# Performance work log

Hardware: AMD Instinct MI355X
Metric: run time of the kernel (lower is better)

The kernel has to match this reference:

```python
import jax, jax.numpy as jnp
import numpy as np

N_NODES = 50000
N_EDGES = 800000
D = 256


def _mean_aggregate(x, src, tgt, num_nodes):
    # scatter-mean of source features onto target nodes: [N, D]
    summed = jax.ops.segment_sum(x[src], tgt, num_segments=num_nodes)
    count = jax.ops.segment_sum(jnp.ones((src.shape[0],), x.dtype), tgt,
                                num_segments=num_nodes)
    return summed / jnp.maximum(count, 1.0)[:, None]


def _sage_conv(x, src, tgt, W_l, b, W_r):
    # PyG SAGEConv (aggr='mean'): lin_l(mean_j x_j) + lin_r(x_i)
    agg = _mean_aggregate(x, src, tgt, x.shape[0])
    return agg @ W_l + b + x @ W_r


def setup_inputs() -> dict:
    key = jax.random.key(0)
    ks = jax.random.split(key, 8)
    s = 1.0 / np.sqrt(D)
    x = jax.random.normal(ks[0], (N_NODES, D), dtype=jnp.float32)
    edge_index = jax.random.randint(ks[1], (2, N_EDGES), 0, N_NODES, dtype=jnp.int64)
    return {
        "x": x,
        "edge_index": edge_index,
        "W1_l": jax.random.normal(ks[2], (D, D), dtype=jnp.float32) * s,
        "b1": jnp.zeros((D,), dtype=jnp.float32),
        "W1_r": jax.random.normal(ks[3], (D, D), dtype=jnp.float32) * s,
        "W2_l": jax.random.normal(ks[4], (D, D), dtype=jnp.float32) * s,
        "b2": jnp.zeros((D,), dtype=jnp.float32),
        "W2_r": jax.random.normal(ks[5], (D, D), dtype=jnp.float32) * s,
    }


def reference(x, edge_index, W1_l, b1, W1_r, W2_l, b2, W2_r):
    src, tgt = edge_index[0], edge_index[1]
    h = jax.nn.relu(_sage_conv(x, src, tgt, W1_l, b1, W1_r))
    return _sage_conv(h, src, tgt, W2_l, b2, W2_r)
```

## Files before the change

### kernel.cpp

```cpp
#include <hip/hip_runtime.h>
#include <hip/hip_bf16.h>

#define NN 50000
#define NE 800000
#define DD 256
#define KK 512
#define PAD 64
#define CSTR 16

#define FB 3125
#define CB 12500
#define WB 1024

typedef unsigned short u16;
typedef unsigned int   u32;
typedef unsigned char  u8;
typedef __attribute__((ext_vector_type(8))) __bf16 bf16x8;
typedef __attribute__((ext_vector_type(4))) float  f32x4;
typedef __attribute__((ext_vector_type(2))) float  f32x2;
typedef __attribute__((ext_vector_type(8))) u16    u16x8;
typedef __attribute__((ext_vector_type(4))) u16    u16x4;

#define GLOAD_LDS16(g, l) \
  __builtin_amdgcn_global_load_lds((const __attribute__((address_space(1))) void*)(g), \
                                   (__attribute__((address_space(3))) void*)(l), 16, 0, 0)

static __device__ __forceinline__ u16 f2bf(float f) {
  u32 u = __float_as_uint(f);
  u32 r = (u + 0x7FFFu + ((u >> 16) & 1u)) >> 16;
  return (u16)r;
}
static __device__ __forceinline__ float bf2f(u16 h) {
  return __uint_as_float(((u32)h) << 16);
}

__global__ void k_prep(const int* __restrict__ src, const int* __restrict__ tgt,
                       int* __restrict__ cnt, int* __restrict__ col,
                       const float* __restrict__ x, u16* __restrict__ x_bf,
                       u32* __restrict__ x_f8,
                       const float* __restrict__ W1l, const float* __restrict__ W1r,
                       const float* __restrict__ W2l, const float* __restrict__ W2r,
                       u16* __restrict__ Wc1T, u16* __restrict__ Wc2T) {
  const int b = blockIdx.x;
  if (b < FB) {
    int i = b * 256 + threadIdx.x;
    int t = tgt[i];
    int p = atomicAdd(&cnt[t * CSTR], 1);
    if (p < PAD) col[t * PAD + p] = src[i];
  } else if (b < FB + CB) {
    int i = (b - FB) * 256 + threadIdx.x;
    const float4 v = *reinterpret_cast<const float4*>(x + i * 4);
    u16x4 o; o.x = f2bf(v.x); o.y = f2bf(v.y); o.z = f2bf(v.z); o.w = f2bf(v.w);
    *reinterpret_cast<u16x4*>(x_bf + i * 4) = o;
    int pk = __builtin_amdgcn_cvt_pk_fp8_f32(v.x, v.y, 0, false);
    pk = __builtin_amdgcn_cvt_pk_fp8_f32(v.z, v.w, pk, true);
    x_f8[i] = (u32)pk;
  } else {
    int gid = (b - FB - CB) * 256 + threadIdx.x;
    int layer = gid >> 17;
    int idx = gid & 131071;
    int n = idx >> 9, k = idx & 511;
    const float* Wl = layer ? W2l : W1l;
    const float* Wr = layer ? W2r : W1r;
    u16* WcT = layer ? Wc2T : Wc1T;
    float v = (k < DD) ? Wl[k * DD + n] : Wr[(k - DD) * DD + n];
    int reg = k >> 6, ko = k & 63;
    int k2 = (reg << 6) + ((((ko >> 3) ^ (n & 7)) << 3)) + (ko & 7);
    WcT[n * KK + k2] = f2bf(v);
  }
}

__global__ void k_aggregate(const u8* __restrict__ feat8, const int* __restrict__ cnt,
                            const int* __restrict__ col, u16* __restrict__ out) {
  const int wave = threadIdx.x >> 6;
  const int lane = threadIdx.x & 63;
  const int half = lane >> 5;
  const int l32 = lane & 31;
  const int node = blockIdx.x * 4 + wave;
  int deg = cnt[node * CSTR];
  if (deg > PAD) deg = PAD;
  const int s = node * PAD, e = s + deg;
  const int fo = l32 * 8;
  float a[8] = {0.f, 0.f, 0.f, 0.f, 0.f, 0.f, 0.f, 0.f};

#define ACC8(vv)                                                       \
  {                                                                    \
    f32x2 p0 = __builtin_amdgcn_cvt_pk_f32_fp8((int)(vv).x, false);    \
    f32x2 p1 = __builtin_amdgcn_cvt_pk_f32_fp8((int)(vv).x, true);     \
    f32x2 p2 = __builtin_amdgcn_cvt_pk_f32_fp8((int)(vv).y, false);    \
    f32x2 p3 = __builtin_amdgcn_cvt_pk_f32_fp8((int)(vv).y, true);     \
    a[0] += p0.x; a[1] += p0.y; a[2] += p1.x; a[3] += p1.y;            \
    a[4] += p2.x; a[5] += p2.y; a[6] += p3.x; a[7] += p3.y;            \
  }

  int i = s + half;
  for (; i + 6 < e; i += 8) {
    int c0 = col[i], c1 = col[i + 2], c2 = col[i + 4], c3 = col[i + 6];
    uint2 v0 = *reinterpret_cast<const uint2*>(feat8 + c0 * DD + fo);
    uint2 v1 = *reinterpret_cast<const uint2*>(feat8 + c1 * DD + fo);
    uint2 v2 = *reinterpret_cast<const uint2*>(feat8 + c2 * DD + fo);
    uint2 v3 = *reinterpret_cast<const uint2*>(feat8 + c3 * DD + fo);
    ACC8(v0) ACC8(v1) ACC8(v2) ACC8(v3)
  }
  for (; i < e; i += 2) {
    uint2 v = *reinterpret_cast<const uint2*>(feat8 + col[i] * DD + fo);
    ACC8(v)
  }
#undef ACC8
#pragma unroll
  for (int j = 0; j < 8; ++j) a[j] += __shfl_xor(a[j], 32, 64);

  if (half == 0) {
    const float scale = (deg > 0) ? 1.0f / (float)deg : 0.0f;
    u16x8 o;
#pragma unroll
    for (int j = 0; j < 8; ++j) o[j] = f2bf(a[j] * scale);
    *reinterpret_cast<u16x8*>(out + node * DD + fo) = o;
  }
}

#define BM 64
#define BN 256
#define BK 64

template <int LAYER>
__global__ void k_gemm_fused(const u16* __restrict__ A0, const u16* __restrict__ A1,
                             const u16* __restrict__ WcT, const float* __restrict__ bias,
                             u16* __restrict__ outb, u8* __restrict__ outf8,
                             float* __restrict__ outf, int M) {
  __shared__ alignas(16) u16 lA[BM * BK];
  __shared__ alignas(16) u16 lB[BN * BK];
  const int tid = threadIdx.x;
  const int rowBase = blockIdx.x * BM;
  const int wave = tid >> 6, lane = tid & 63;
  const int wc = wave;
  const int l8 = lane >> 3;
  const int ch = lane & 7;

  f32x4 acc[4][4] = {};

  for (int k0 = 0; k0 < KK; k0 += BK) {
    if (k0) __syncthreads();
    const u16* Asrc = (k0 < DD) ? A0 : A1;
    const int kk = k0 & (DD - 1);
#pragma unroll
    for (int j = 0; j < 2; ++j) {
      int row = wave * 16 + j * 8 + l8;
      const u16* g = Asrc + (size_t)(rowBase + row) * DD + kk + ((ch ^ (row & 7)) << 3);
      GLOAD_LDS16(g, &lA[(wave * 16 + j * 8) * BK]);
    }
#pragma unroll
    for (int j = 0; j < 8; ++j) {
      int row = wave * 64 + j * 8 + l8;
      const u16* g = WcT + (size_t)row * KK + k0 + (ch << 3);
      GLOAD_LDS16(g, &lB[(wave * 64 + j * 8) * BK]);
    }
    __syncthreads();

#pragma unroll
    for (int ks = 0; ks < 2; ++ks) {
      const int kbyte = ks * 64 + (lane >> 4) * 16;
      bf16x8 af[4], bfg[4];
#pragma unroll
      for (int m = 0; m < 4; ++m) {
        int row = m * 16 + (lane & 15);
        af[m] = *reinterpret_cast<const bf16x8*>((const char*)lA + row * 128 + (kbyte ^ ((row & 7) << 4)));
      }
#pragma unroll
      for (int n = 0; n < 4; ++n) {
        int row = wc * 64 + n * 16 + (lane & 15);
        bfg[n] = *reinterpret_cast<const bf16x8*>((const char*)lB + row * 128 + (kbyte ^ ((row & 7) << 4)));
      }
#pragma unroll
      for (int m = 0; m < 4; ++m)
#pragma unroll
        for (int n = 0; n < 4; ++n)
          acc[m][n] = __builtin_amdgcn_mfma_f32_16x16x32_bf16(af[m], bfg[n], acc[m][n], 0, 0, 0);
    }
  }

  const int lrow = (lane >> 4) * 4;
  const int lcol = lane & 15;
#pragma unroll
  for (int n = 0; n < 4; ++n) {
    const int gcol = wc * 64 + n * 16 + lcol;
    const float bv = bias[gcol];
#pragma unroll
    for (int m = 0; m < 4; ++m) {
#pragma unroll
      for (int r = 0; r < 4; ++r) {
        const int grow = rowBase + m * 16 + lrow + r;
        if (grow < M) {
          float v = acc[m][n][r] + bv;
          if (LAYER == 1) {
            v = fmaxf(v, 0.0f);
            outb[grow * DD + gcol] = f2bf(v);
            int pk = __builtin_amdgcn_cvt_pk_fp8_f32(v, 0.0f, 0, false);
            outf8[grow * DD + gcol] = (u8)(pk & 0xff);
          } else {
            outf[grow * DD + gcol] = v;
          }
        }
      }
    }
  }
}

extern "C" void kernel_launch(void* const* d_in, const int* in_sizes, int n_in,
                              void* d_out, int out_size, void* d_ws, size_t ws_size,
                              hipStream_t stream) {
  const float* x    = (const float*)d_in[0];
  const int*   ei   = (const int*)d_in[1];
  const float* W1l  = (const float*)d_in[2];
  const float* b1   = (const float*)d_in[3];
  const float* W1r  = (const float*)d_in[4];
  const float* W2l  = (const float*)d_in[5];
  const float* b2   = (const float*)d_in[6];
  const float* W2r  = (const float*)d_in[7];
  float* out = (float*)d_out;

  const int* srcIdx = ei;
  const int* tgtIdx = ei + NE;

  char* ws = (char*)d_ws;
  int* cnt    = (int*)(ws + 0);
  int* col    = (int*)(ws + 3200000);
  u16* x_bf   = (u16*)(ws + 16000000);
  u16* h_bf   = (u16*)(ws + 41600000);
  u16* agg_bf = (u16*)(ws + 67200000);
  u8*  x_f8   = (u8*) (ws + 92800000);
  u8*  h_f8   = (u8*) (ws + 105600000);
  u16* Wc1T   = (u16*)(ws + 118400000);
  u16* Wc2T   = (u16*)(ws + 118662144);

  hipMemsetAsync(cnt, 0, NN * CSTR * sizeof(int), stream);
  k_prep<<<FB + CB + WB, 256, 0, stream>>>(srcIdx, tgtIdx, cnt, col, x, x_bf,
                                           (u32*)x_f8,
                                           W1l, W1r, W2l, W2r, Wc1T, Wc2T);

  const int ggrid = (NN + BM - 1) / BM;

  k_aggregate<<<NN / 4, 256, 0, stream>>>(x_f8, cnt, col, agg_bf);
  k_gemm_fused<1><<<ggrid, 256, 0, stream>>>(agg_bf, x_bf, Wc1T, b1, h_bf, h_f8, nullptr, NN);
  k_aggregate<<<NN / 4, 256, 0, stream>>>(h_f8, cnt, col, agg_bf);
  k_gemm_fused<2><<<ggrid, 256, 0, stream>>>(agg_bf, h_bf, Wc2T, b2, nullptr, nullptr, out, NN);
}
```

Measured before the change: 199.6 us.

## Bucket edges by target range then build padded CSR with LDS atomics

Replaces the per-edge global atomic on a strided count array with a two-pass bucketing scheme. Edges are first binned into 7 target-range buckets, each split into 32 replicas, using wave-aggregated atomics. A new 56-block kernel then scans its bucket's replicas and fills the padded adjacency using shared-memory counters. This removes 800k contended global atomics and the large memset. The cost is an extra kernel launch, an extra write and read of an 8-byte edge buffer, and each build block rescanning its whole bucket. Segment capacity overflow could silently drop edges if the distribution is skewed.

```diff
diff --git a/kernel.cpp b/kernel.cpp
--- a/kernel.cpp
+++ b/kernel.cpp
@@ -6,7 +6,11 @@
 #define DD 256
 #define KK 512
 #define PAD 64
-#define CSTR 16
+
+#define NBUCK 7
+#define BSH 13
+#define REPL 32
+#define SEGCAP 5120
 
 #define FB 3125
 #define CB 12500
@@ -15,6 +19,7 @@
 typedef unsigned short u16;
 typedef unsigned int   u32;
 typedef unsigned char  u8;
+typedef unsigned long long u64;
 typedef __attribute__((ext_vector_type(8))) __bf16 bf16x8;
 typedef __attribute__((ext_vector_type(4))) float  f32x4;
 typedef __attribute__((ext_vector_type(2))) float  f32x2;
@@ -30,12 +35,9 @@
   u32 r = (u + 0x7FFFu + ((u >> 16) & 1u)) >> 16;
   return (u16)r;
 }
-static __device__ __forceinline__ float bf2f(u16 h) {
-  return __uint_as_float(((u32)h) << 16);
-}
 
 __global__ void k_prep(const int* __restrict__ src, const int* __restrict__ tgt,
-                       int* __restrict__ cnt, int* __restrict__ col,
+                       int* __restrict__ cur, u64* __restrict__ ebuf,
                        const float* __restrict__ x, u16* __restrict__ x_bf,
                        u32* __restrict__ x_f8,
                        const float* __restrict__ W1l, const float* __restrict__ W1r,
@@ -43,10 +45,25 @@
                        u16* __restrict__ Wc1T, u16* __restrict__ Wc2T) {
   const int b = blockIdx.x;
   if (b < FB) {
-    int i = b * 256 + threadIdx.x;
-    int t = tgt[i];
-    int p = atomicAdd(&cnt[t * CSTR], 1);
-    if (p < PAD) col[t * PAD + p] = src[i];
+    const int i = b * 256 + threadIdx.x;
+    const int lane = threadIdx.x & 63;
+    const int t = tgt[i], s = src[i];
+    const int bk = t >> BSH;
+    const int rep = b & (REPL - 1);
+    const u64 rec = ((u64)(u32)s << 32) | (u32)t;
+#pragma unroll
+    for (int q = 0; q < NBUCK; ++q) {
+      u64 m = __ballot(bk == q);
+      if (bk == q) {
+        int leader = __ffsll((unsigned long long)m) - 1;
+        int base = 0;
+        if (lane == leader) base = atomicAdd(&cur[(q * REPL + rep) * 16], (int)__popcll(m));
+        base = __shfl(base, leader, 64);
+        int my = base + (int)__popcll(m & ((1ull << lane) - 1ull));
+        if (my < SEGCAP)
+          ebuf[(size_t)(q * REPL + rep) * SEGCAP + my] = rec;
+      }
+    }
   } else if (b < FB + CB) {
     int i = (b - FB) * 256 + threadIdx.x;
     const float4 v = *reinterpret_cast<const float4*>(x + i * 4);
@@ -70,6 +87,35 @@
   }
 }
 
+__global__ void k_build(const int* __restrict__ cur, const u64* __restrict__ ebuf,
+                        int* __restrict__ cnt, int* __restrict__ col) {
+  __shared__ int lcnt[1024];
+  const int w = blockIdx.x;
+  const int bk = w >> 3, sub = w & 7;
+  const int n0 = (bk << BSH) + (sub << 10);
+  const int n1 = min(n0 + 1024, NN);
+  lcnt[threadIdx.x] = 0;
+  __syncthreads();
+  if (n0 < NN) {
+    for (int g = 0; g < REPL; ++g) {
+      const int sN = min(cur[(bk * REPL + g) * 16], SEGCAP);
+      const u64* seg = ebuf + (size_t)(bk * REPL + g) * SEGCAP;
+      for (int j = threadIdx.x; j < sN; j += 1024) {
+        u64 e = seg[j];
+        int t = (int)(u32)(e & 0xffffffffull);
+        if (t >= n0 && t < n1) {
+          int s = (int)(e >> 32);
+          int p = atomicAdd(&lcnt[t - n0], 1);
+          if (p < PAD) col[t * PAD + p] = s;
+        }
+      }
+    }
+  }
+  __syncthreads();
+  const int n = n0 + threadIdx.x;
+  if (n < n1) cnt[n] = lcnt[threadIdx.x];
+}
+
 __global__ void k_aggregate(const u8* __restrict__ feat8, const int* __restrict__ cnt,
                             const int* __restrict__ col, u16* __restrict__ out) {
   const int wave = threadIdx.x >> 6;
@@ -77,7 +123,7 @@
   const int half = lane >> 5;
   const int l32 = lane & 31;
   const int node = blockIdx.x * 4 + wave;
-  int deg = cnt[node * CSTR];
+  int deg = cnt[node];
   if (deg > PAD) deg = PAD;
   const int s = node * PAD, e = s + deg;
   const int fo = l32 * 8;
@@ -223,20 +269,23 @@
   const int* tgtIdx = ei + NE;
 
   char* ws = (char*)d_ws;
-  int* cnt    = (int*)(ws + 0);
-  int* col    = (int*)(ws + 3200000);
-  u16* x_bf   = (u16*)(ws + 16000000);
-  u16* h_bf   = (u16*)(ws + 41600000);
-  u16* agg_bf = (u16*)(ws + 67200000);
-  u8*  x_f8   = (u8*) (ws + 92800000);
-  u8*  h_f8   = (u8*) (ws + 105600000);
-  u16* Wc1T   = (u16*)(ws + 118400000);
-  u16* Wc2T   = (u16*)(ws + 118662144);
-
-  hipMemsetAsync(cnt, 0, NN * CSTR * sizeof(int), stream);
-  k_prep<<<FB + CB + WB, 256, 0, stream>>>(srcIdx, tgtIdx, cnt, col, x, x_bf,
+  int* cur    = (int*)(ws + 0);
+  int* cnt    = (int*)(ws + 14336);
+  int* col    = (int*)(ws + 214400);
+  u64* ebuf   = (u64*)(ws + 13014400);
+  u16* x_bf   = (u16*)(ws + 22189440);
+  u16* h_bf   = (u16*)(ws + 47789440);
+  u16* agg_bf = (u16*)(ws + 73389440);
+  u8*  x_f8   = (u8*) (ws + 98989440);
+  u8*  h_f8   = (u8*) (ws + 111789440);
+  u16* Wc1T   = (u16*)(ws + 124589440);
+  u16* Wc2T   = (u16*)(ws + 124851584);
+
+  hipMemsetAsync(cur, 0, NBUCK * REPL * 16 * sizeof(int), stream);
+  k_prep<<<FB + CB + WB, 256, 0, stream>>>(srcIdx, tgtIdx, cur, ebuf, x, x_bf,
                                            (u32*)x_f8,
                                            W1l, W1r, W2l, W2r, Wc1T, Wc2T);
+  k_build<<<56, 1024, 0, stream>>>(cur, ebuf, cnt, col);
 
   const int ggrid = (NN + BM - 1) / BM;
 
```

Measured after the change: 237.3 us. +18.9%, slower.
